# Kernel optimization log

Measured on AMD Instinct MI355X. Metric: run time of the kernel, lower is better.

Reference implementation:

```python
import jax, jax.numpy as jnp
import numpy as np

N = 2_097_152          # sampled points
H = 16                 # hash heads / levels
F = 2                  # features per head
M = 524_288            # 2**19 table size
HID = 64               # mlp width
OUT = 3


def setup_inputs() -> dict:
    key = jax.random.key(0)
    ks = jax.random.split(key, 12)
    idx = jax.random.randint(ks[0], (N, H), 0, M, dtype=jnp.int64)
    tables = jax.random.normal(ks[1], (H, M, F), dtype=jnp.float32) * 0.02
    d_in = H * F  # 32
    def lin(k, d1, d2):
        kw, kb = jax.random.split(k)
        s = 1.0 / np.sqrt(d1)
        W = jax.random.uniform(kw, (d1, d2), jnp.float32, -s, s)
        b = jax.random.uniform(kb, (d2,), jnp.float32, -s, s)
        return W, b
    W1, b1 = lin(ks[2], d_in, HID)
    W2, b2 = lin(ks[3], HID, HID)
    W3, b3 = lin(ks[4], HID, HID)
    W4, b4 = lin(ks[5], HID, OUT)
    return {"idx": idx, "tables": tables,
            "W1": W1, "b1": b1, "W2": W2, "b2": b2,
            "W3": W3, "b3": b3, "W4": W4, "b4": b4}


def reference(idx, tables, W1, b1, W2, b2, W3, b3, W4, b4):
    # per-head gather: tables[h][idx[:, h]] -> [N, H, F], then concat heads
    gather = jax.vmap(lambda t, i: t[i], in_axes=(0, 1), out_axes=1)
    x = gather(tables, idx).reshape(idx.shape[0], -1)  # [N, H*F]
    x = jax.nn.relu(x @ W1 + b1)
    x = jax.nn.relu(x @ W2 + b2)
    x = jax.nn.relu(x @ W3 + b3)
    return x @ W4 + b4  # [N, 3]
```

## Files before the change

### kernel.cpp

```cpp
#include <hip/hip_runtime.h>
#include <hip/hip_bf16.h>

typedef __attribute__((ext_vector_type(8))) short short8;
typedef __attribute__((ext_vector_type(4))) float floatx4;
typedef __attribute__((ext_vector_type(4))) int int4v;
typedef __attribute__((ext_vector_type(4))) unsigned int uint4v;

#define MTBL 524288
#define HSTRIDE 72

union U4S8 { uint4v u; short8 s; };

static __device__ __forceinline__ unsigned int pack2bf(float a, float b) {
    union { float f; unsigned int u; } x, y;
    x.f = a; y.f = b;
    unsigned int lo = (x.u + 0x8000u) >> 16;
    unsigned int hi = (y.u + 0x8000u) & 0xFFFF0000u;
    return lo | hi;
}
static __device__ __forceinline__ short bf1(float a) {
    union { float f; unsigned int u; } x;
    x.f = a;
    return (short)((x.u + 0x8000u) >> 16);
}

static __device__ __forceinline__ short8 relu_pack(floatx4 a, floatx4 b) {
    union { __hip_bfloat162 h2[4]; short8 s; } r;
    r.h2[0] = __float22bfloat162_rn(make_float2(fmaxf(a[0], 0.f), fmaxf(a[1], 0.f)));
    r.h2[1] = __float22bfloat162_rn(make_float2(fmaxf(a[2], 0.f), fmaxf(a[3], 0.f)));
    r.h2[2] = __float22bfloat162_rn(make_float2(fmaxf(b[0], 0.f), fmaxf(b[1], 0.f)));
    r.h2[3] = __float22bfloat162_rn(make_float2(fmaxf(b[2], 0.f), fmaxf(b[3], 0.f)));
    return r.s;
}

static __device__ __forceinline__ floatx4 mlp_chain(
    uint4v cur,
    const short8 (&A1)[4], const short8 (&A2)[4][2], const short8 (&A3)[4][2],
    const short8 (&A4)[2],
    const floatx4 (&C1)[4], const floatx4 (&C2)[4], const floatx4 (&C3)[4],
    floatx4 C4)
{
    U4S8 bx; bx.u = cur;
    const short8 Bx = bx.s;

    floatx4 h[4];
#pragma unroll
    for (int t = 0; t < 4; ++t)
        h[t] = __builtin_amdgcn_mfma_f32_16x16x32_bf16(A1[t], Bx, C1[t], 0, 0, 0);
    short8 B0 = relu_pack(h[0], h[1]);
    short8 B1 = relu_pack(h[2], h[3]);

#pragma unroll
    for (int t = 0; t < 4; ++t) {
        h[t] = __builtin_amdgcn_mfma_f32_16x16x32_bf16(A2[t][0], B0, C2[t], 0, 0, 0);
        h[t] = __builtin_amdgcn_mfma_f32_16x16x32_bf16(A2[t][1], B1, h[t], 0, 0, 0);
    }
    B0 = relu_pack(h[0], h[1]);
    B1 = relu_pack(h[2], h[3]);

#pragma unroll
    for (int t = 0; t < 4; ++t) {
        h[t] = __builtin_amdgcn_mfma_f32_16x16x32_bf16(A3[t][0], B0, C3[t], 0, 0, 0);
        h[t] = __builtin_amdgcn_mfma_f32_16x16x32_bf16(A3[t][1], B1, h[t], 0, 0, 0);
    }
    B0 = relu_pack(h[0], h[1]);
    B1 = relu_pack(h[2], h[3]);

    floatx4 o;
    o = __builtin_amdgcn_mfma_f32_16x16x32_bf16(A4[0], B0, C4, 0, 0, 0);
    o = __builtin_amdgcn_mfma_f32_16x16x32_bf16(A4[1], B1, o, 0, 0, 0);
    return o;
}

__global__ __launch_bounds__(256) void ngp_prep(
    const int* __restrict__ idx, int* __restrict__ idxT,
    const floatx4* __restrict__ tab4, unsigned int* __restrict__ tblC, int N)
{
    const int tblocks = N >> 10;
    if ((int)blockIdx.x < tblocks) {
        const int t  = blockIdx.x * 256 + threadIdx.x;
        const int p0 = t * 4;
        const int4v* rows = (const int4v*)idx;
        int4v r[4][4];
#pragma unroll
        for (int p = 0; p < 4; ++p)
#pragma unroll
            for (int c = 0; c < 4; ++c)
                r[p][c] = rows[(size_t)(p0 + p) * 4 + c];
#pragma unroll
        for (int c = 0; c < 4; ++c)
#pragma unroll
            for (int k = 0; k < 4; ++k) {
                const int h = c * 4 + k;
                int4v w;
                w[0] = r[0][c][k]; w[1] = r[1][c][k]; w[2] = r[2][c][k]; w[3] = r[3][c][k];
                __builtin_nontemporal_store(w, (int4v*)(idxT + (size_t)h * N + p0));
            }
    } else {
        const int t = (blockIdx.x - tblocks) * 256 + threadIdx.x;
        floatx4 a = tab4[(size_t)2 * t];
        floatx4 b = tab4[(size_t)2 * t + 1];
        uint4v w;
        w[0] = pack2bf(a[0], a[1]);
        w[1] = pack2bf(a[2], a[3]);
        w[2] = pack2bf(b[0], b[1]);
        w[3] = pack2bf(b[2], b[3]);
        __builtin_nontemporal_store(w, (uint4v*)(tblC + (size_t)4 * t));
    }
}

__global__ __launch_bounds__(256) void ngp_gather(
    const int* __restrict__ idxT, const unsigned int* __restrict__ tblC,
    unsigned int* __restrict__ xU, int N, int iters)
{
    const int phase = (blockIdx.x >> 11) & 1;
    const int blk   = blockIdx.x & 2047;
    const int h     = ((blk & 7) << 1) | phase;
    const int slot  = blk >> 3;
    const int* __restrict__ ih = idxT + (size_t)h * N;
    const unsigned int* __restrict__ th = tblC + (size_t)h * MTBL;
    unsigned int* __restrict__ xh = xU + (size_t)h * N;

    int p = slot * (N >> 8) + (threadIdx.x << 2);
    int4v iv0 = __builtin_nontemporal_load((const int4v*)(ih + p));
    int4v iv1 = __builtin_nontemporal_load((const int4v*)(ih + p + 1024));
    for (int it = 0; it < iters; ++it) {
        int4v nv0 = iv0, nv1 = iv1;
        if (it + 1 < iters) {
            nv0 = __builtin_nontemporal_load((const int4v*)(ih + p + 2048));
            nv1 = __builtin_nontemporal_load((const int4v*)(ih + p + 3072));
        }
        uint4v w0, w1;
        w0[0] = th[iv0[0]]; w0[1] = th[iv0[1]]; w0[2] = th[iv0[2]]; w0[3] = th[iv0[3]];
        w1[0] = th[iv1[0]]; w1[1] = th[iv1[1]]; w1[2] = th[iv1[2]]; w1[3] = th[iv1[3]];
        __builtin_nontemporal_store(w0, (uint4v*)(xh + p));
        __builtin_nontemporal_store(w1, (uint4v*)(xh + p + 1024));
        iv0 = nv0; iv1 = nv1;
        p += 2048;
    }
}

__global__ __launch_bounds__(256, 2) void ngp_mlp(
    const unsigned int* __restrict__ xU,
    const float* __restrict__ W1, const float* __restrict__ b1,
    const float* __restrict__ W2, const float* __restrict__ b2,
    const float* __restrict__ W3, const float* __restrict__ b3,
    const float* __restrict__ W4, const float* __restrict__ b4,
    float* __restrict__ out, int N, int tiles_per_wave)
{
    __shared__ float sW[6144];

    const int tid  = threadIdx.x;
    const int wave = tid >> 6;
    const int lane = tid & 63;
    const int q = lane >> 4;
    const int m = lane & 15;

    int ct[4];
#pragma unroll
    for (int t = 0; t < 4; ++t)
        ct[t] = 32 * (t >> 1) + 4 * (t & 1) + 8 * (m >> 2) + (m & 3);

    short8 A1[4], A2[4][2], A3[4][2], A4[2];
    floatx4 C1[4], C2[4], C3[4], C4;

    for (int i = tid; i < 2048; i += 256) sW[i] = W1[i];
    for (int i = tid; i < 4096; i += 256) sW[2048 + i] = W2[i];
    __syncthreads();
#pragma unroll
    for (int t = 0; t < 4; ++t) {
        short8 a;
#pragma unroll
        for (int j = 0; j < 8; ++j)
            a[j] = bf1(sW[(q * 8 + j) * 64 + ct[t]]);
        A1[t] = a;
    }
#pragma unroll
    for (int t = 0; t < 4; ++t)
#pragma unroll
        for (int c = 0; c < 2; ++c) {
            short8 a;
#pragma unroll
            for (int j = 0; j < 8; ++j)
                a[j] = bf1(sW[2048 + (c * 32 + q * 8 + j) * 64 + ct[t]]);
            A2[t][c] = a;
        }
    __syncthreads();

    for (int i = tid; i < 4096; i += 256) sW[i] = W3[i];
    if (tid < 192) sW[4096 + tid] = W4[tid];
    if (tid < 64)       sW[4288 + tid] = b1[tid];
    else if (tid < 128) sW[4288 + tid] = b2[tid - 64];
    else if (tid < 192) sW[4288 + tid] = b3[tid - 128];
    else if (tid < 195) sW[4288 + tid] = b4[tid - 192];
    __syncthreads();
#pragma unroll
    for (int t = 0; t < 4; ++t)
#pragma unroll
        for (int c = 0; c < 2; ++c) {
            short8 a;
#pragma unroll
            for (int j = 0; j < 8; ++j)
                a[j] = bf1(sW[(c * 32 + q * 8 + j) * 64 + ct[t]]);
            A3[t][c] = a;
        }
#pragma unroll
    for (int c = 0; c < 2; ++c) {
        short8 a;
#pragma unroll
        for (int j = 0; j < 8; ++j)
            a[j] = (m < 3) ? bf1(sW[4096 + (c * 32 + q * 8 + j) * 3 + m]) : (short)0;
        A4[c] = a;
    }
#pragma unroll
    for (int t = 0; t < 4; ++t) {
        const int bi = 32 * (t >> 1) + 4 * (t & 1) + 8 * q;
#pragma unroll
        for (int r = 0; r < 4; ++r) {
            C1[t][r] = sW[4288 + bi + r];
            C2[t][r] = sW[4288 + 64 + bi + r];
            C3[t][r] = sW[4288 + 128 + bi + r];
        }
    }
#pragma unroll
    for (int r = 0; r < 4; ++r)
        C4[r] = (q == 0 && r < 3) ? sW[4288 + 192 + r] : 0.0f;

    const int gw = blockIdx.x * 4 + wave;
    const int tile0 = gw * tiles_per_wave;
    const int iters = tiles_per_wave >> 1;

    const unsigned int* xr = xU + (size_t)(q * 4) * N + m;

    #define XLD(tile, c) __builtin_nontemporal_load(&xr[(size_t)(c) * N + (tile) * 16])

    uint4v curA, curB;
    {
        curA[0] = XLD(tile0, 0);     curA[1] = XLD(tile0, 1);
        curA[2] = XLD(tile0, 2);     curA[3] = XLD(tile0, 3);
        curB[0] = XLD(tile0 + 1, 0); curB[1] = XLD(tile0 + 1, 1);
        curB[2] = XLD(tile0 + 1, 2); curB[3] = XLD(tile0 + 1, 3);
    }

    for (int k = 0; k < iters; ++k) {
        const int pbaseA = (tile0 + 2 * k) * 16;
        const bool more = (k + 1) < iters;

        uint4v nxtA = curA, nxtB = curB;
        if (more) {
            const int tn = tile0 + 2 * k + 2;
            nxtA[0] = XLD(tn, 0);     nxtA[1] = XLD(tn, 1);
            nxtA[2] = XLD(tn, 2);     nxtA[3] = XLD(tn, 3);
            nxtB[0] = XLD(tn + 1, 0); nxtB[1] = XLD(tn + 1, 1);
            nxtB[2] = XLD(tn + 1, 2); nxtB[3] = XLD(tn + 1, 3);
        }

        floatx4 oA = mlp_chain(curA, A1, A2, A3, A4, C1, C2, C3, C4);
        floatx4 oB = mlp_chain(curB, A1, A2, A3, A4, C1, C2, C3, C4);

        if (q == 0) {
            const int pA = pbaseA + m;
            __builtin_nontemporal_store(oA[0], out + pA * 3 + 0);
            __builtin_nontemporal_store(oA[1], out + pA * 3 + 1);
            __builtin_nontemporal_store(oA[2], out + pA * 3 + 2);
            const int pB = pA + 16;
            __builtin_nontemporal_store(oB[0], out + pB * 3 + 0);
            __builtin_nontemporal_store(oB[1], out + pB * 3 + 1);
            __builtin_nontemporal_store(oB[2], out + pB * 3 + 2);
        }

        curA = nxtA;
        curB = nxtB;
    }
    #undef XLD
}

__global__ __launch_bounds__(256, 2) void ngp_fused(
    const int* __restrict__ idx,
    const float* __restrict__ tables,
    const float* __restrict__ W1, const float* __restrict__ b1,
    const float* __restrict__ W2, const float* __restrict__ b2,
    const float* __restrict__ W3, const float* __restrict__ b3,
    const float* __restrict__ W4, const float* __restrict__ b4,
    float* __restrict__ out, int tiles_per_wave)
{
    __shared__ float sW1[2048];
    __shared__ float sW2[4096];
    __shared__ float sW3[4096];
    __shared__ float sW4[192];
    __shared__ float sB[200];
    __shared__ __hip_bfloat16 sH[4][16 * HSTRIDE];

    const int tid = threadIdx.x;
    for (int i = tid; i < 2048; i += 256) sW1[i] = W1[i];
    for (int i = tid; i < 4096; i += 256) sW2[i] = W2[i];
    for (int i = tid; i < 4096; i += 256) sW3[i] = W3[i];
    if (tid < 192) sW4[tid] = W4[tid];
    if (tid < 64)       sB[tid] = b1[tid];
    else if (tid < 128) sB[tid] = b2[tid - 64];
    else if (tid < 192) sB[tid] = b3[tid - 128];
    else if (tid < 195) sB[tid] = b4[tid - 192];
    __syncthreads();

    const int wave = tid >> 6;
    const int lane = tid & 63;
    const int q = lane >> 4;
    const int m = lane & 15;

    short8 A1[4], A2[4][2], A3[4][2], A4[2];
#pragma unroll
    for (int t = 0; t < 4; ++t) {
        short8 a;
#pragma unroll
        for (int j = 0; j < 8; ++j)
            a[j] = bf1(sW1[(q * 8 + j) * 64 + t * 16 + m]);
        A1[t] = a;
    }
#pragma unroll
    for (int t = 0; t < 4; ++t)
#pragma unroll
        for (int c = 0; c < 2; ++c) {
            short8 a, a3;
#pragma unroll
            for (int j = 0; j < 8; ++j) {
                a[j]  = bf1(sW2[(c * 32 + q * 8 + j) * 64 + t * 16 + m]);
                a3[j] = bf1(sW3[(c * 32 + q * 8 + j) * 64 + t * 16 + m]);
            }
            A2[t][c] = a;
            A3[t][c] = a3;
        }
#pragma unroll
    for (int c = 0; c < 2; ++c) {
        short8 a;
#pragma unroll
        for (int j = 0; j < 8; ++j)
            a[j] = (m < 3) ? bf1(sW4[(c * 32 + q * 8 + j) * 3 + m]) : (short)0;
        A4[c] = a;
    }

    floatx4 C1[4], C2[4], C3[4], C4;
#pragma unroll
    for (int t = 0; t < 4; ++t)
#pragma unroll
        for (int r = 0; r < 4; ++r) {
            C1[t][r] = sB[t * 16 + q * 4 + r];
            C2[t][r] = sB[64 + t * 16 + q * 4 + r];
            C3[t][r] = sB[128 + t * 16 + q * 4 + r];
        }
#pragma unroll
    for (int r = 0; r < 4; ++r)
        C4[r] = (q == 0 && r < 3) ? sB[192 + r] : 0.0f;

    __hip_bfloat16* hrow = &sH[wave][m * HSTRIDE];
    const int4*   idx4 = (const int4*)idx;
    const float2* tbl  = (const float2*)tables;

    const int gw = blockIdx.x * 4 + wave;
    const int tile0 = gw * tiles_per_wave;

    int4 iv = idx4[(tile0 * 16 + m) * 4 + q];
    float2 g0 = tbl[(q * 4 + 0) * MTBL + iv.x];
    float2 g1 = tbl[(q * 4 + 1) * MTBL + iv.y];
    float2 g2 = tbl[(q * 4 + 2) * MTBL + iv.z];
    float2 g3 = tbl[(q * 4 + 3) * MTBL + iv.w];

    for (int it = 0; it < tiles_per_wave; ++it) {
        const int pbase = (tile0 + it) * 16;
        const bool more = (it + 1) < tiles_per_wave;

        short8 Bx;
        {
            unsigned int p0 = pack2bf(g0.x, g0.y);
            unsigned int p1 = pack2bf(g1.x, g1.y);
            unsigned int p2 = pack2bf(g2.x, g2.y);
            unsigned int p3 = pack2bf(g3.x, g3.y);
            Bx[0] = (short)(p0 & 0xFFFF); Bx[1] = (short)(p0 >> 16);
            Bx[2] = (short)(p1 & 0xFFFF); Bx[3] = (short)(p1 >> 16);
            Bx[4] = (short)(p2 & 0xFFFF); Bx[5] = (short)(p2 >> 16);
            Bx[6] = (short)(p3 & 0xFFFF); Bx[7] = (short)(p3 >> 16);
        }

        int4 ivn;
        if (more) ivn = idx4[((pbase + 16) + m) * 4 + q];

        floatx4 acc[4];
#pragma unroll
        for (int t = 0; t < 4; ++t)
            acc[t] = __builtin_amdgcn_mfma_f32_16x16x32_bf16(A1[t], Bx, C1[t], 0, 0, 0);

#pragma unroll
        for (int t = 0; t < 4; ++t) {
            uint2 pk;
            pk.x = pack2bf(fmaxf(acc[t][0], 0.f), fmaxf(acc[t][1], 0.f));
            pk.y = pack2bf(fmaxf(acc[t][2], 0.f), fmaxf(acc[t][3], 0.f));
            *(uint2*)(hrow + t * 16 + q * 4) = pk;
        }
        short8 Bh0 = *(const short8*)(hrow + q * 8);
        short8 Bh1 = *(const short8*)(hrow + 32 + q * 8);

#pragma unroll
        for (int t = 0; t < 4; ++t) {
            acc[t] = __builtin_amdgcn_mfma_f32_16x16x32_bf16(A2[t][0], Bh0, C2[t], 0, 0, 0);
            acc[t] = __builtin_amdgcn_mfma_f32_16x16x32_bf16(A2[t][1], Bh1, acc[t], 0, 0, 0);
        }

        if (more) {
            g0 = tbl[(q * 4 + 0) * MTBL + ivn.x];
            g1 = tbl[(q * 4 + 1) * MTBL + ivn.y];
            g2 = tbl[(q * 4 + 2) * MTBL + ivn.z];
            g3 = tbl[(q * 4 + 3) * MTBL + ivn.w];
        }

#pragma unroll
        for (int t = 0; t < 4; ++t) {
            uint2 pk;
            pk.x = pack2bf(fmaxf(acc[t][0], 0.f), fmaxf(acc[t][1], 0.f));
            pk.y = pack2bf(fmaxf(acc[t][2], 0.f), fmaxf(acc[t][3], 0.f));
            *(uint2*)(hrow + t * 16 + q * 4) = pk;
        }
        Bh0 = *(const short8*)(hrow + q * 8);
        Bh1 = *(const short8*)(hrow + 32 + q * 8);

#pragma unroll
        for (int t = 0; t < 4; ++t) {
            acc[t] = __builtin_amdgcn_mfma_f32_16x16x32_bf16(A3[t][0], Bh0, C3[t], 0, 0, 0);
            acc[t] = __builtin_amdgcn_mfma_f32_16x16x32_bf16(A3[t][1], Bh1, acc[t], 0, 0, 0);
        }

#pragma unroll
        for (int t = 0; t < 4; ++t) {
            uint2 pk;
            pk.x = pack2bf(fmaxf(acc[t][0], 0.f), fmaxf(acc[t][1], 0.f));
            pk.y = pack2bf(fmaxf(acc[t][2], 0.f), fmaxf(acc[t][3], 0.f));
            *(uint2*)(hrow + t * 16 + q * 4) = pk;
        }
        Bh0 = *(const short8*)(hrow + q * 8);
        Bh1 = *(const short8*)(hrow + 32 + q * 8);

        floatx4 o;
        o = __builtin_amdgcn_mfma_f32_16x16x32_bf16(A4[0], Bh0, C4, 0, 0, 0);
        o = __builtin_amdgcn_mfma_f32_16x16x32_bf16(A4[1], Bh1, o, 0, 0, 0);

        if (q == 0) {
            const int pn = pbase + m;
            out[pn * 3 + 0] = o[0];
            out[pn * 3 + 1] = o[1];
            out[pn * 3 + 2] = o[2];
        }
    }
}

extern "C" void kernel_launch(void* const* d_in, const int* in_sizes, int n_in,
                              void* d_out, int out_size, void* d_ws, size_t ws_size,
                              hipStream_t stream) {
    const int*   idx    = (const int*)d_in[0];
    const float* tables = (const float*)d_in[1];
    const float* W1 = (const float*)d_in[2];
    const float* b1 = (const float*)d_in[3];
    const float* W2 = (const float*)d_in[4];
    const float* b2 = (const float*)d_in[5];
    const float* W3 = (const float*)d_in[6];
    const float* b3 = (const float*)d_in[7];
    const float* W4 = (const float*)d_in[8];
    const float* b4 = (const float*)d_in[9];
    float* out = (float*)d_out;

    const int N = in_sizes[0] / 16;
    const int total_tiles = N / 16;

    const size_t idxT_bytes = (size_t)16 * N * 4;
    const size_t xU_bytes   = (size_t)16 * N * 4;
    const size_t tblC_bytes = (size_t)16 * MTBL * 4;
    const size_t need = idxT_bytes + xU_bytes + tblC_bytes;

    if (ws_size >= need) {
        int*          idxT = (int*)d_ws;
        unsigned int* xU   = (unsigned int*)((char*)d_ws + idxT_bytes);
        unsigned int* tblC = (unsigned int*)((char*)d_ws + idxT_bytes + xU_bytes);

        const int tblocks = N / 1024;
        const int cblocks = (16 * MTBL) / 1024;
        ngp_prep<<<tblocks + cblocks, 256, 0, stream>>>(
            idx, idxT, (const floatx4*)tables, tblC, N);
        const int iters = (N >> 8) >> 11;
        ngp_gather<<<4096, 256, 0, stream>>>(idxT, tblC, xU, N, iters);
        const int blocks = 4096;
        const int tiles_per_wave = total_tiles / (blocks * 4);
        ngp_mlp<<<blocks, 256, 0, stream>>>(xU, W1, b1, W2, b2, W3, b3, W4, b4,
                                            out, N, tiles_per_wave);
    } else {
        const int blocks = 2048;
        const int tiles_per_wave = total_tiles / (blocks * 4);
        ngp_fused<<<blocks, 256, 0, stream>>>(idx, tables, W1, b1, W2, b2, W3, b3,
                                              W4, b4, out, tiles_per_wave);
    }
}
```

Baseline: 567.5 us.

## Transpose idx via LDS in prep and deepen MLP prefetch pipeline

The index transpose in the prep kernel now stages a 512-point tile in padded LDS, so both the global reads and the per-head writes are fully coalesced. Before, each thread did strided row reads and wrote only 4 contiguous points per head. The MLP kernel now keeps loads for three tile-pairs in flight instead of one, and its grid is halved so each wave processes more tiles. The deeper prefetch uses more registers, which may reduce occupancy. The table conversion also switches to nontemporal loads.

```diff
diff --git a/kernel.cpp b/kernel.cpp
--- a/kernel.cpp
+++ b/kernel.cpp
@@ -76,30 +76,39 @@
     const int* __restrict__ idx, int* __restrict__ idxT,
     const floatx4* __restrict__ tab4, unsigned int* __restrict__ tblC, int N)
 {
-    const int tblocks = N >> 10;
+    __shared__ int lds[512 * 17];
+    const int tblocks = N >> 9;
+    const int tid = threadIdx.x;
     if ((int)blockIdx.x < tblocks) {
-        const int t  = blockIdx.x * 256 + threadIdx.x;
-        const int p0 = t * 4;
-        const int4v* rows = (const int4v*)idx;
-        int4v r[4][4];
-#pragma unroll
-        for (int p = 0; p < 4; ++p)
-#pragma unroll
-            for (int c = 0; c < 4; ++c)
-                r[p][c] = rows[(size_t)(p0 + p) * 4 + c];
-#pragma unroll
-        for (int c = 0; c < 4; ++c)
-#pragma unroll
-            for (int k = 0; k < 4; ++k) {
-                const int h = c * 4 + k;
-                int4v w;
-                w[0] = r[0][c][k]; w[1] = r[1][c][k]; w[2] = r[2][c][k]; w[3] = r[3][c][k];
-                __builtin_nontemporal_store(w, (int4v*)(idxT + (size_t)h * N + p0));
-            }
+        const int P = blockIdx.x << 9;
+        const int4v* rows = (const int4v*)idx + (size_t)P * 4;
+#pragma unroll
+        for (int c = 0; c < 8; ++c) {
+            const int g = tid + 256 * c;
+            int4v v = __builtin_nontemporal_load(rows + g);
+            const int lp = g >> 2;
+            const int h0 = (g & 3) * 4;
+#pragma unroll
+            for (int j = 0; j < 4; ++j)
+                lds[lp * 17 + h0 + j] = v[j];
+        }
+        __syncthreads();
+#pragma unroll
+        for (int c = 0; c < 8; ++c) {
+            const int g = tid + 256 * c;
+            const int h = g >> 7;
+            const int po4 = g & 127;
+            int4v w;
+#pragma unroll
+            for (int j = 0; j < 4; ++j)
+                w[j] = lds[(4 * po4 + j) * 17 + h];
+            __builtin_nontemporal_store(
+                w, (int4v*)(idxT + (size_t)h * N + P + 4 * po4));
+        }
     } else {
-        const int t = (blockIdx.x - tblocks) * 256 + threadIdx.x;
-        floatx4 a = tab4[(size_t)2 * t];
-        floatx4 b = tab4[(size_t)2 * t + 1];
+        const int t = (blockIdx.x - tblocks) * 256 + tid;
+        floatx4 a = __builtin_nontemporal_load(tab4 + (size_t)2 * t);
+        floatx4 b = __builtin_nontemporal_load(tab4 + (size_t)2 * t + 1);
         uint4v w;
         w[0] = pack2bf(a[0], a[1]);
         w[1] = pack2bf(a[2], a[3]);
@@ -233,33 +242,26 @@
     const unsigned int* xr = xU + (size_t)(q * 4) * N + m;
 
     #define XLD(tile, c) __builtin_nontemporal_load(&xr[(size_t)(c) * N + (tile) * 16])
-
-    uint4v curA, curB;
-    {
-        curA[0] = XLD(tile0, 0);     curA[1] = XLD(tile0, 1);
-        curA[2] = XLD(tile0, 2);     curA[3] = XLD(tile0, 3);
-        curB[0] = XLD(tile0 + 1, 0); curB[1] = XLD(tile0 + 1, 1);
-        curB[2] = XLD(tile0 + 1, 2); curB[3] = XLD(tile0 + 1, 3);
-    }
+    #define LDP(A, B, tile) \
+        A[0] = XLD(tile, 0);       A[1] = XLD(tile, 1); \
+        A[2] = XLD(tile, 2);       A[3] = XLD(tile, 3); \
+        B[0] = XLD((tile) + 1, 0); B[1] = XLD((tile) + 1, 1); \
+        B[2] = XLD((tile) + 1, 2); B[3] = XLD((tile) + 1, 3);
+
+    uint4v pa0, pb0, pa1, pb1, pa2, pb2, pa3, pb3;
+    LDP(pa0, pb0, tile0);
+    if (iters > 1) { LDP(pa1, pb1, tile0 + 2); } else { pa1 = pa0; pb1 = pb0; }
+    if (iters > 2) { LDP(pa2, pb2, tile0 + 4); } else { pa2 = pa1; pb2 = pb1; }
+    pa3 = pa2; pb3 = pb2;
 
     for (int k = 0; k < iters; ++k) {
-        const int pbaseA = (tile0 + 2 * k) * 16;
-        const bool more = (k + 1) < iters;
-
-        uint4v nxtA = curA, nxtB = curB;
-        if (more) {
-            const int tn = tile0 + 2 * k + 2;
-            nxtA[0] = XLD(tn, 0);     nxtA[1] = XLD(tn, 1);
-            nxtA[2] = XLD(tn, 2);     nxtA[3] = XLD(tn, 3);
-            nxtB[0] = XLD(tn + 1, 0); nxtB[1] = XLD(tn + 1, 1);
-            nxtB[2] = XLD(tn + 1, 2); nxtB[3] = XLD(tn + 1, 3);
-        }
-
-        floatx4 oA = mlp_chain(curA, A1, A2, A3, A4, C1, C2, C3, C4);
-        floatx4 oB = mlp_chain(curB, A1, A2, A3, A4, C1, C2, C3, C4);
+        if (k + 3 < iters) { LDP(pa3, pb3, tile0 + 2 * k + 6); }
+
+        floatx4 oA = mlp_chain(pa0, A1, A2, A3, A4, C1, C2, C3, C4);
+        floatx4 oB = mlp_chain(pb0, A1, A2, A3, A4, C1, C2, C3, C4);
 
         if (q == 0) {
-            const int pA = pbaseA + m;
+            const int pA = (tile0 + 2 * k) * 16 + m;
             __builtin_nontemporal_store(oA[0], out + pA * 3 + 0);
             __builtin_nontemporal_store(oA[1], out + pA * 3 + 1);
             __builtin_nontemporal_store(oA[2], out + pA * 3 + 2);
@@ -269,9 +271,11 @@
             __builtin_nontemporal_store(oB[2], out + pB * 3 + 2);
         }
 
-        curA = nxtA;
-        curB = nxtB;
-    }
+        pa0 = pa1; pb0 = pb1;
+        pa1 = pa2; pb1 = pb2;
+        pa2 = pa3; pb2 = pb3;
+    }
+    #undef LDP
     #undef XLD
 }
 
@@ -478,13 +482,13 @@
         unsigned int* xU   = (unsigned int*)((char*)d_ws + idxT_bytes);
         unsigned int* tblC = (unsigned int*)((char*)d_ws + idxT_bytes + xU_bytes);
 
-        const int tblocks = N / 1024;
+        const int tblocks = N / 512;
         const int cblocks = (16 * MTBL) / 1024;
         ngp_prep<<<tblocks + cblocks, 256, 0, stream>>>(
             idx, idxT, (const floatx4*)tables, tblC, N);
         const int iters = (N >> 8) >> 11;
         ngp_gather<<<4096, 256, 0, stream>>>(idxT, tblC, xU, N, iters);
-        const int blocks = 4096;
+        const int blocks = 2048;
         const int tiles_per_wave = total_tiles / (blocks * 4);
         ngp_mlp<<<blocks, 256, 0, stream>>>(xU, W1, b1, W2, b2, W3, b3, W4, b4,
                                             out, N, tiles_per_wave);
```

New measurement: 537.6 us. 5.3% less time.
